# Kernel tuning notes

Measured on AMD Instinct MI355X. Metric: run time of the kernel, lower is better.

The kernel has to match this reference:

```python
import jax, jax.numpy as jnp
import numpy as np
from jax import lax

DN = ('NCHW', 'OIHW', 'NCHW')
BETA = 0.25


def _conv(x, w, b, stride, pad):
    y = lax.conv_general_dilated(x, w, (stride, stride), [(pad, pad), (pad, pad)],
                                 dimension_numbers=DN)
    return y + b[None, :, None, None]


def _convT(x, w, b, stride, pad, opad):
    # torch ConvTranspose2d(w: [in,out,kh,kw]) == dilated conv with flipped, transposed kernel
    k = w.shape[2]
    wf = jnp.transpose(w, (1, 0, 2, 3))[:, :, ::-1, ::-1]
    lo = k - 1 - pad
    hi = k - 1 - pad + opad
    y = lax.conv_general_dilated(x, wf, (1, 1), [(lo, hi), (lo, hi)],
                                 lhs_dilation=(stride, stride), dimension_numbers=DN)
    return y + b[None, :, None, None]


def setup_inputs() -> dict:
    key = jax.random.key(0)
    ks = jax.random.split(key, 16)
    s = 0.05
    inp = {
        'x': jax.random.normal(ks[0], (64, 3, 125, 125), jnp.float32),
        'enc_w1': jax.random.normal(ks[1], (32, 3, 3, 3), jnp.float32) * s,
        'enc_b1': jnp.zeros((32,), jnp.float32),
        'enc_w2': jax.random.normal(ks[2], (64, 32, 3, 3), jnp.float32) * s,
        'enc_b2': jnp.zeros((64,), jnp.float32),
        'enc_w3': jax.random.normal(ks[3], (64, 64, 1, 1), jnp.float32) * s,
        'enc_b3': jnp.zeros((64,), jnp.float32),
        'codebook': jax.random.normal(ks[4], (512, 64), jnp.float32),
        'dec_w1': jax.random.normal(ks[5], (64, 64, 3, 3), jnp.float32) * s,  # torch [in,out,kh,kw]
        'dec_b1': jnp.zeros((64,), jnp.float32),
        'dec_w2': jax.random.normal(ks[6], (64, 32, 3, 3), jnp.float32) * s,
        'dec_b2': jnp.zeros((32,), jnp.float32),
        'dec_w3': jax.random.normal(ks[7], (32, 3, 2, 2), jnp.float32) * s,
        'dec_b3': jnp.zeros((3,), jnp.float32),
    }
    return inp


def reference(x, enc_w1, enc_b1, enc_w2, enc_b2, enc_w3, enc_b3, codebook,
              dec_w1, dec_b1, dec_w2, dec_b2, dec_w3, dec_b3):
    # Encoder
    z = jax.nn.relu(_conv(x, enc_w1, enc_b1, 2, 1))
    z = jax.nn.relu(_conv(z, enc_w2, enc_b2, 2, 1))
    z = _conv(z, enc_w3, enc_b3, 1, 0)  # [B, D, h, w]

    # VQ (training mode)
    zp = jnp.transpose(z, (0, 2, 3, 1))  # [B, h, w, D]
    flat = zp.reshape(-1, zp.shape[-1])  # [N, D]
    d = (jnp.sum(flat * flat, axis=1, keepdims=True)
         + jnp.sum(codebook * codebook, axis=1)
         - 2.0 * flat @ codebook.T)  # [N, K]
    idx = jnp.argmin(d, axis=1)
    q = codebook[idx].reshape(zp.shape)

    q_latent_loss = jnp.mean((q - lax.stop_gradient(zp)) ** 2)
    e_latent_loss = jnp.mean((zp - lax.stop_gradient(q)) ** 2)
    e_q_loss = q_latent_loss + BETA * e_latent_loss

    q_st = zp + lax.stop_gradient(q - zp)  # straight-through
    e = jnp.transpose(q_st, (0, 3, 1, 2))

    # Decoder
    h = jax.nn.relu(_convT(e, dec_w1, dec_b1, 2, 1, 1))
    h = jax.nn.relu(_convT(h, dec_w2, dec_b2, 2, 1, 1))
    x_recon = _convT(h, dec_w3, dec_b3, 1, 2, 0)

    recon_loss = jnp.sum((x_recon - x) ** 2)
    loss_sum = e_q_loss + recon_loss
    return (loss_sum, e_q_loss, recon_loss, x_recon)
```

## Files before the change

### kernel.cpp

```cpp
#include <hip/hip_runtime.h>

#define DEV __device__ __forceinline__
typedef unsigned short u16;
typedef __bf16 bf16x8 __attribute__((ext_vector_type(8)));
typedef float f32x4 __attribute__((ext_vector_type(4)));

DEV u16 f2bf(float f) {
  unsigned u = __float_as_uint(f);
  u += 0x7FFF + ((u >> 16) & 1);
  return (u16)(u >> 16);
}


__global__ __launch_bounds__(256) void k_prep(
    const float* __restrict__ ew1, const float* __restrict__ ew2,
    const float* __restrict__ ew3, const float* __restrict__ dw1,
    const float* __restrict__ dw2, const float* __restrict__ dw3,
    const float* __restrict__ cb,
    float* __restrict__ wc1p, float* __restrict__ wc3p,
    u16* __restrict__ w3f, float* __restrict__ c2,
    u16* __restrict__ w2f, u16* __restrict__ wt1f, u16* __restrict__ wt2f,
    u16* __restrict__ cbf) {
  int i = blockIdx.x * 256 + threadIdx.x;
  if (i < 864) {
    int cl = i & 7; int t = i >> 3; int tap = t % 9; t /= 9; int ci = t % 3; int cog = t / 3;
    wc1p[i] = ew1[((cog * 8 + cl) * 3 + ci) * 9 + tap];
  } else if (i < 4960) {
    int j = i - 864; int cl = j & 7; int t = j >> 3; int ci = t & 63; int cog = t >> 6;
    wc3p[j] = ew3[(cog * 8 + cl) * 64 + ci];
  } else if (i < 9056) {
    int j = i - 4960;
    int jj = j & 7; int lane = (j >> 3) & 63; int tp = (j >> 9) & 3; int hl = j >> 11;
    int kh = tp >> 1, kw = tp & 1;
    int ci = ((lane >> 4) << 3) + jj; int co = lane & 15;
    float wv = (co < 3) ? dw3[((ci * 3 + co) * 2 + kh) * 2 + kw] : 0.f;
    u16 hi = f2bf(wv);
    if (hl == 0) w3f[j] = hi;
    else         w3f[j] = f2bf(wv - __uint_as_float((unsigned)hi << 16));
  } else if (i < 9568) {
    int k = i - 9056;
    const float4* c4 = (const float4*)(cb + (k << 6));
    float s = 0.f;
    #pragma unroll
    for (int q = 0; q < 16; ++q) { float4 v = c4[q]; s += v.x*v.x + v.y*v.y + v.z*v.z + v.w*v.w; }
    c2[k] = s;
  } else if (i < 28000) {
    int j = i - 9568;
    int jj = j & 7; int lane = (j >> 3) & 63; int nf = (j >> 9) & 3; int kt = j >> 11;
    int kh = kt / 3, kw = kt % 3;
    int ci = ((lane >> 4) << 3) + jj; int co = (nf << 4) + (lane & 15);
    w2f[j] = f2bf(ew2[((co * 32 + ci) * 3 + kh) * 3 + kw]);
  } else if (i < 64864) {
    int j = i - 28000;
    int jj = j & 7; int lane = (j >> 3) & 63; int nf = (j >> 9) & 3; int s = (j >> 11) & 1; int kt = j >> 12;
    int kh = kt / 3, kw = kt % 3;
    int ci = (s << 5) + ((lane >> 4) << 3) + jj; int co = (nf << 4) + (lane & 15);
    wt1f[j] = f2bf(dw1[((ci * 64 + co) * 3 + kh) * 3 + kw]);
  } else if (i < 83296) {
    int j = i - 64864;
    int jj = j & 7; int lane = (j >> 3) & 63; int nf = (j >> 9) & 1; int s = (j >> 10) & 1; int kt = j >> 11;
    int kh = kt / 3, kw = kt % 3;
    int ci = (s << 5) + ((lane >> 4) << 3) + jj; int co = (nf << 4) + (lane & 15);
    wt2f[j] = f2bf(dw2[((ci * 32 + co) * 3 + kh) * 3 + kw]);
  } else if (i < 148832) {
    int j = i - 83296;
    int jj = j & 7; int lane = (j >> 3) & 63; int nt = (j >> 9) & 31; int ks = (j >> 14) & 1; int hl = j >> 15;
    int ci = (ks << 5) + ((lane >> 4) << 3) + jj;
    int code = (nt << 4) + (lane & 15);
    float v = cb[(code << 6) + ci];
    u16 hi = f2bf(v);
    cbf[j] = hl ? f2bf(v - __uint_as_float((unsigned)hi << 16)) : hi;
  }
}

__global__ __launch_bounds__(256) void k_pad(
    const float* __restrict__ x, float* __restrict__ xp) {
  int idx = blockIdx.x * 256 + threadIdx.x;
  int c4 = idx & 31;
  int r  = (idx >> 5) % 129;
  int cbp = (idx >> 5) / 129;
  int ih = r - 1;
  float4 v = make_float4(0.f, 0.f, 0.f, 0.f);
  if ((unsigned)ih < 125u) {
    const float* rp = x + (cbp * 125 + ih) * 125;
    int iw0 = c4 * 4 - 1;
    if (iw0 >= 0)        v.x = rp[iw0];
    if (iw0 + 1 < 125)   v.y = rp[iw0 + 1];
    if (iw0 + 2 < 125)   v.z = rp[iw0 + 2];
    if (iw0 + 3 < 125)   v.w = rp[iw0 + 3];
  }
  *(float4*)(xp + (cbp * 129 + r) * 128 + c4 * 4) = v;
}

__global__ __launch_bounds__(256) void k_conv1(
    const float* __restrict__ xp, const float* __restrict__ wp,
    const float* __restrict__ bias, u16* __restrict__ z1t) {
  __shared__ u16 st[256 * 34];
  int t = threadIdx.x;
  int slab = blockIdx.x & 15, b = blockIdx.x >> 4;
  int tx = t & 15, ty = (t >> 4) & 3, cg = t >> 6;
  int oh = slab * 4 + ty;
  int co0 = cg * 8;
  const float* wcg = wp + cg * 216;
  float acc[8][4];
  #pragma unroll
  for (int c = 0; c < 8; ++c) {
    float bv = bias[co0 + c];
    #pragma unroll
    for (int s = 0; s < 4; ++s) acc[c][s] = bv;
  }
  #pragma unroll
  for (int ci = 0; ci < 3; ++ci) {
    #pragma unroll
    for (int kh = 0; kh < 3; ++kh) {
      const float* rp = xp + ((b * 3 + ci) * 129 + (2 * oh + kh)) * 128 + 8 * tx;
      float4 qa = *(const float4*)rp;
      float4 qb = *(const float4*)(rp + 4);
      float v8 = rp[8];
      float v[9] = {qa.x, qa.y, qa.z, qa.w, qb.x, qb.y, qb.z, qb.w, v8};
      #pragma unroll
      for (int kw = 0; kw < 3; ++kw) {
        const float* wq = wcg + (ci * 9 + kh * 3 + kw) * 8;
        float4 wa = *(const float4*)wq;
        float4 wb = *(const float4*)(wq + 4);
        float w8[8] = {wa.x, wa.y, wa.z, wa.w, wb.x, wb.y, wb.z, wb.w};
        #pragma unroll
        for (int s = 0; s < 4; ++s) {
          float in = v[2 * s + kw];
          #pragma unroll
          for (int c = 0; c < 8; ++c) acc[c][s] = fmaf(in, w8[c], acc[c][s]);
        }
      }
    }
  }
  #pragma unroll
  for (int s = 0; s < 4; ++s) {
    bool wok = (tx * 4 + s) < 63;
    unsigned p0 = 0, p1 = 0, p2 = 0, p3 = 0;
    if (wok) {
      p0 = f2bf(fmaxf(acc[0][s], 0.f)) | ((unsigned)f2bf(fmaxf(acc[1][s], 0.f)) << 16);
      p1 = f2bf(fmaxf(acc[2][s], 0.f)) | ((unsigned)f2bf(fmaxf(acc[3][s], 0.f)) << 16);
      p2 = f2bf(fmaxf(acc[4][s], 0.f)) | ((unsigned)f2bf(fmaxf(acc[5][s], 0.f)) << 16);
      p3 = f2bf(fmaxf(acc[6][s], 0.f)) | ((unsigned)f2bf(fmaxf(acc[7][s], 0.f)) << 16);
    }
    int lpix = tx * 16 + ty * 4 + s;
    *(uint4*)&st[lpix * 34 + co0] = make_uint4(p0, p1, p2, p3);
  }
  __syncthreads();
  {
    int p = t;
    int ow = (p >> 4) * 4 + (p & 3);
    int ohl = (p >> 2) & 3;
    int oho = slab * 4 + ohl;
    if (oho < 63) {
      const u16* lp = &st[p * 34];
      uint4 a0 = *(const uint4*)(lp);
      uint4 a1 = *(const uint4*)(lp + 8);
      uint4 a2 = *(const uint4*)(lp + 16);
      uint4 a3 = *(const uint4*)(lp + 24);
      uint4* gp = (uint4*)(z1t + ((b * 63 + oho) * 64 + ow) * 32);
      gp[0] = a0; gp[1] = a1; gp[2] = a2; gp[3] = a3;
    }
  }
}

__global__ __launch_bounds__(256) void k_conv2(
    const u16* __restrict__ z1t, const u16* __restrict__ wf,
    const float* __restrict__ bias, float* __restrict__ z2) {
  int t = threadIdx.x;
  int lane = t & 63, wv = t >> 6;
  int n = lane & 15, q = lane >> 4;
  int raw = blockIdx.x;
  int wg = ((raw & 7) << 8) + (raw >> 3);
  int oh = wg & 31, b = wg >> 5;
  int xt = wv & 1, ch = wv >> 1;
  int xA = xt * 16 + n;
  f32x4 acc[2] = {{0,0,0,0},{0,0,0,0}};
  #pragma unroll
  for (int kh = 0; kh < 3; ++kh) {
    int ih = 2 * oh - 1 + kh;
    bool yok = (unsigned)ih < 63u;
    #pragma unroll
    for (int kw = 0; kw < 3; ++kw) {
      int iw = 2 * xA - 1 + kw;
      bool ok = yok && (iw >= 0);
      bf16x8 a = {};
      if (ok) a = *(const bf16x8*)(z1t + ((b * 63 + ih) * 64 + iw) * 32 + q * 8);
      int kt = kh * 3 + kw;
      const u16* wb = wf + ((kt << 2) + (ch << 1)) * 512 + lane * 8;
      bf16x8 b0 = *(const bf16x8*)wb;
      bf16x8 b1 = *(const bf16x8*)(wb + 512);
      acc[0] = __builtin_amdgcn_mfma_f32_16x16x32_bf16(a, b0, acc[0], 0, 0, 0);
      acc[1] = __builtin_amdgcn_mfma_f32_16x16x32_bf16(a, b1, acc[1], 0, 0, 0);
    }
  }
  #pragma unroll
  for (int j = 0; j < 2; ++j) {
    int co = ((ch << 1) + j) * 16 + n;
    float bv = bias[co];
    float4 rv = make_float4(fmaxf(acc[j][0] + bv, 0.f), fmaxf(acc[j][1] + bv, 0.f),
                            fmaxf(acc[j][2] + bv, 0.f), fmaxf(acc[j][3] + bv, 0.f));
    *(float4*)(z2 + ((b * 64 + co) * 32 + oh) * 32 + xt * 16 + q * 4) = rv;
  }
}

__global__ __launch_bounds__(256) void k_conv3(
    const float* __restrict__ in, const float* __restrict__ wp,
    const float* __restrict__ bias, float* __restrict__ z3,
    u16* __restrict__ z3h, u16* __restrict__ z3l) {
  __shared__ u16 lh[128 * 72];
  __shared__ u16 ll[128 * 72];
  int t = threadIdx.x;
  int pxg = blockIdx.x & 7; int b = blockIdx.x >> 3;
  int pxi = t & 31, cog = t >> 5;
  int px0 = pxg * 128 + pxi * 4;
  const float* wcg = wp + cog * 512;
  int co0 = cog * 8;
  float acc[8][4];
  #pragma unroll
  for (int c = 0; c < 8; ++c) {
    float bv = bias[co0 + c];
    #pragma unroll
    for (int s = 0; s < 4; ++s) acc[c][s] = bv;
  }
  const float* ip = in + (b << 16) + px0;
  for (int ci = 0; ci < 64; ++ci) {
    float4 v = *(const float4*)(ip + (ci << 10));
    float4 wa = *(const float4*)(wcg + ci * 8);
    float4 wb = *(const float4*)(wcg + ci * 8 + 4);
    float w8[8] = {wa.x, wa.y, wa.z, wa.w, wb.x, wb.y, wb.z, wb.w};
    #pragma unroll
    for (int c = 0; c < 8; ++c) {
      acc[c][0] = fmaf(v.x, w8[c], acc[c][0]);
      acc[c][1] = fmaf(v.y, w8[c], acc[c][1]);
      acc[c][2] = fmaf(v.z, w8[c], acc[c][2]);
      acc[c][3] = fmaf(v.w, w8[c], acc[c][3]);
    }
  }
  float* op = z3 + ((b << 6) + co0) * 1024 + px0;
  #pragma unroll
  for (int c = 0; c < 8; ++c)
    *(float4*)(op + (c << 10)) = make_float4(acc[c][0], acc[c][1], acc[c][2], acc[c][3]);
  #pragma unroll
  for (int s = 0; s < 4; ++s) {
    unsigned h[4], l[4];
    #pragma unroll
    for (int g = 0; g < 4; ++g) {
      float v0 = acc[2 * g][s], v1 = acc[2 * g + 1][s];
      u16 h0 = f2bf(v0), h1 = f2bf(v1);
      u16 l0 = f2bf(v0 - __uint_as_float((unsigned)h0 << 16));
      u16 l1 = f2bf(v1 - __uint_as_float((unsigned)h1 << 16));
      h[g] = h0 | ((unsigned)h1 << 16);
      l[g] = l0 | ((unsigned)l1 << 16);
    }
    int la = (pxi * 4 + s) * 72 + co0;
    *(uint4*)&lh[la] = make_uint4(h[0], h[1], h[2], h[3]);
    *(uint4*)&ll[la] = make_uint4(l[0], l[1], l[2], l[3]);
  }
  __syncthreads();
  {
    int p = t >> 1, half = t & 1;
    int la = p * 72 + half * 32;
    uint4 h0 = *(uint4*)&lh[la],      h1 = *(uint4*)&lh[la + 8];
    uint4 h2 = *(uint4*)&lh[la + 16], h3 = *(uint4*)&lh[la + 24];
    uint4 l0 = *(uint4*)&ll[la],      l1 = *(uint4*)&ll[la + 8];
    uint4 l2 = *(uint4*)&ll[la + 16], l3 = *(uint4*)&ll[la + 24];
    long gp = ((long)b * 1024 + pxg * 128 + p) * 64 + half * 32;
    uint4* oh = (uint4*)(z3h + gp);
    uint4* ol = (uint4*)(z3l + gp);
    oh[0] = h0; oh[1] = h1; oh[2] = h2; oh[3] = h3;
    ol[0] = l0; ol[1] = l1; ol[2] = l2; ol[3] = l3;
  }
}

__global__ __launch_bounds__(256) void k_vqp(
    const u16* __restrict__ z3h, const u16* __restrict__ z3l,
    const u16* __restrict__ cbf, const float* __restrict__ c2v,
    int* __restrict__ idxb) {
  int t = threadIdx.x;
  int lane = t & 63, wv = t >> 6;
  int n = lane & 15, q = lane >> 4;
  int p0 = blockIdx.x * 64;
  bf16x8 Ah[4][2], Al[4][2];
  #pragma unroll
  for (int mt = 0; mt < 4; ++mt) {
    const u16* ap = z3h + (p0 + mt * 16 + n) * 64 + q * 8;
    const u16* al = z3l + (p0 + mt * 16 + n) * 64 + q * 8;
    Ah[mt][0] = *(const bf16x8*)ap;  Ah[mt][1] = *(const bf16x8*)(ap + 32);
    Al[mt][0] = *(const bf16x8*)al;  Al[mt][1] = *(const bf16x8*)(al + 32);
  }
  float bs[4][4]; int bix[4][4];
  #pragma unroll
  for (int mt = 0; mt < 4; ++mt)
    #pragma unroll
    for (int r = 0; r < 4; ++r) { bs[mt][r] = 3.4e38f; bix[mt][r] = 0; }
  #pragma unroll
  for (int nt0 = 0; nt0 < 8; ++nt0) {
    int nt = wv * 8 + nt0;
    const u16* bp = cbf + lane * 8;
    bf16x8 Bh0 = *(const bf16x8*)(bp + (nt << 9));
    bf16x8 Bh1 = *(const bf16x8*)(bp + ((32 + nt) << 9));
    bf16x8 Bl0 = *(const bf16x8*)(bp + ((64 + nt) << 9));
    bf16x8 Bl1 = *(const bf16x8*)(bp + ((96 + nt) << 9));
    float c2 = c2v[(nt << 4) + n];
    #pragma unroll
    for (int mt = 0; mt < 4; ++mt) {
      f32x4 acc = {0.f, 0.f, 0.f, 0.f};
      acc = __builtin_amdgcn_mfma_f32_16x16x32_bf16(Ah[mt][0], Bh0, acc, 0, 0, 0);
      acc = __builtin_amdgcn_mfma_f32_16x16x32_bf16(Ah[mt][1], Bh1, acc, 0, 0, 0);
      acc = __builtin_amdgcn_mfma_f32_16x16x32_bf16(Al[mt][0], Bh0, acc, 0, 0, 0);
      acc = __builtin_amdgcn_mfma_f32_16x16x32_bf16(Al[mt][1], Bh1, acc, 0, 0, 0);
      acc = __builtin_amdgcn_mfma_f32_16x16x32_bf16(Ah[mt][0], Bl0, acc, 0, 0, 0);
      acc = __builtin_amdgcn_mfma_f32_16x16x32_bf16(Ah[mt][1], Bl1, acc, 0, 0, 0);
      int idx = (nt << 4) + n;
      #pragma unroll
      for (int r = 0; r < 4; ++r) {
        float sc = fmaf(-2.f, acc[r], c2);
        if (sc < bs[mt][r]) { bs[mt][r] = sc; bix[mt][r] = idx; }
      }
    }
  }
  #pragma unroll
  for (int off = 8; off > 0; off >>= 1) {
    #pragma unroll
    for (int mt = 0; mt < 4; ++mt)
      #pragma unroll
      for (int r = 0; r < 4; ++r) {
        float os = __shfl_xor(bs[mt][r], off, 16);
        int oi = __shfl_xor(bix[mt][r], off, 16);
        if (os < bs[mt][r] || (os == bs[mt][r] && oi < bix[mt][r])) {
          bs[mt][r] = os; bix[mt][r] = oi;
        }
      }
  }
  __shared__ float ls[4][64];
  __shared__ int   li[4][64];
  if (n == 0) {
    #pragma unroll
    for (int mt = 0; mt < 4; ++mt)
      #pragma unroll
      for (int r = 0; r < 4; ++r) {
        int px = mt * 16 + q * 4 + r;
        ls[wv][px] = bs[mt][r];
        li[wv][px] = bix[mt][r];
      }
  }
  __syncthreads();
  if (t < 64) {
    float best = ls[0][t]; int bi = li[0][t];
    #pragma unroll
    for (int w = 1; w < 4; ++w) {
      float s = ls[w][t]; int ii = li[w][t];
      if (s < best || (s == best && ii < bi)) { best = s; bi = ii; }
    }
    idxb[p0 + t] = bi;
  }
}

__global__ __launch_bounds__(256) void k_vqf(
    const float* __restrict__ z3, const float* __restrict__ cb,
    const int* __restrict__ idxb, u16* __restrict__ et,
    float* __restrict__ acc) {
  int n = blockIdx.x * 256 + threadIdx.x;
  int bi = idxb[n];
  int b = n >> 10, hw = n & 1023;
  const float* zp = z3 + (b << 16) + hw;
  uint2* ep = (uint2*)(et + (n << 6));
  const float4* cq = (const float4*)(cb + (bi << 6));
  float lsum = 0.f;
  #pragma unroll
  for (int i = 0; i < 16; ++i) {
    float4 c = cq[i];
    float zv, df;
    zv = zp[(4*i+0) << 10]; df = c.x - zv; lsum = fmaf(df, df, lsum);
    zv = zp[(4*i+1) << 10]; df = c.y - zv; lsum = fmaf(df, df, lsum);
    zv = zp[(4*i+2) << 10]; df = c.z - zv; lsum = fmaf(df, df, lsum);
    zv = zp[(4*i+3) << 10]; df = c.w - zv; lsum = fmaf(df, df, lsum);
    ep[i] = make_uint2(f2bf(c.x) | ((unsigned)f2bf(c.y) << 16),
                       f2bf(c.z) | ((unsigned)f2bf(c.w) << 16));
  }
  __shared__ float red[256];
  red[threadIdx.x] = lsum; __syncthreads();
  #pragma unroll
  for (int s = 128; s > 0; s >>= 1) {
    if (threadIdx.x < s) red[threadIdx.x] += red[threadIdx.x + s];
    __syncthreads();
  }
  if (threadIdx.x == 0) atomicAdd(acc + 0, red[0]);
}

__global__ __launch_bounds__(256) void k_convT1(
    const u16* __restrict__ et, const u16* __restrict__ wf,
    const float* __restrict__ bias, u16* __restrict__ h1t) {
  __shared__ u16 wl[36 * 512];
  __shared__ u16 st[4][64 * 34];
  int t = threadIdx.x;
  int lane = t & 63, wv = t >> 6;
  int yw = wv & 1, xt = wv >> 1;
  int raw = blockIdx.x;
  int wg = ((raw & 7) << 7) + (raw >> 3);
  int cog = wg & 1;
  int yg = (wg >> 1) & 7;
  int b = wg >> 4;
  {
    const uint4* gw = (const uint4*)wf;
    uint4* lw = (uint4*)wl;
    #pragma unroll
    for (int k = 0; k < 9; ++k) {
      int i = t + 256 * k;
      int slot = i >> 6, within = i & 63;
      int kt = slot >> 2, j = (slot >> 1) & 1, ks = slot & 1;
      int goff = (kt << 12) + (((ks << 2) + (cog << 1) + j) << 9);
      lw[i] = gw[(goff >> 3) + within];
    }
  }
  int n = lane & 15, q = lane >> 4;
  int m = xt * 16 + n;
  __syncthreads();
  for (int iter = 0; iter < 2; ++iter) {
    int y = yg * 4 + iter * 2 + yw;
    const u16* base0 = et + (((b * 32 + y) * 32) << 6) + q * 8;
    bf16x8 P00a, P00b, P01a = {}, P01b = {}, P10a = {}, P10b = {}, P11a = {}, P11b = {};
    { const u16* p = base0 + (m << 6); P00a = *(const bf16x8*)p; P00b = *(const bf16x8*)(p + 32); }
    if (m + 1 < 32) { const u16* p = base0 + ((m + 1) << 6); P01a = *(const bf16x8*)p; P01b = *(const bf16x8*)(p + 32); }
    if (y + 1 < 32) {
      const u16* base1 = base0 + (32 << 6);
      { const u16* p = base1 + (m << 6); P10a = *(const bf16x8*)p; P10b = *(const bf16x8*)(p + 32); }
      if (m + 1 < 32) { const u16* p = base1 + ((m + 1) << 6); P11a = *(const bf16x8*)p; P11b = *(const bf16x8*)(p + 32); }
    }
    f32x4 accE[2][2] = {};
    f32x4 accO[2][2] = {};
    #pragma unroll
    for (int kw = 0; kw < 3; ++kw) {
      int pwi = (kw == 1) ? 0 : 1;
      bf16x8 A0a = (kw == 0) ? P01a : P00a;
      bf16x8 A0b = (kw == 0) ? P01b : P00b;
      bf16x8 A1a = (kw == 0) ? P11a : P10a;
      bf16x8 A1b = (kw == 0) ? P11b : P10b;
      #pragma unroll
      for (int j = 0; j < 2; ++j) {
        const u16* wE  = wl + ((((3 + kw) << 2) + (j << 1)) << 9) + lane * 8;
        const u16* wO0 = wl + (((kw << 2) + (j << 1)) << 9) + lane * 8;
        const u16* wO2 = wl + ((((6 + kw) << 2) + (j << 1)) << 9) + lane * 8;
        bf16x8 bE0 = *(const bf16x8*)wE;
        bf16x8 bE1 = *(const bf16x8*)(wE + 512);
        accE[j][pwi] = __builtin_amdgcn_mfma_f32_16x16x32_bf16(A0a, bE0, accE[j][pwi], 0, 0, 0);
        accE[j][pwi] = __builtin_amdgcn_mfma_f32_16x16x32_bf16(A0b, bE1, accE[j][pwi], 0, 0, 0);
        bf16x8 bO00 = *(const bf16x8*)wO0;
        bf16x8 bO01 = *(const bf16x8*)(wO0 + 512);
        accO[j][pwi] = __builtin_amdgcn_mfma_f32_16x16x32_bf16(A1a, bO00, accO[j][pwi], 0, 0, 0);
        accO[j][pwi] = __builtin_amdgcn_mfma_f32_16x16x32_bf16(A1b, bO01, accO[j][pwi], 0, 0, 0);
        bf16x8 bO20 = *(const bf16x8*)wO2;
        bf16x8 bO21 = *(const bf16x8*)(wO2 + 512);
        accO[j][pwi] = __builtin_amdgcn_mfma_f32_16x16x32_bf16(A0a, bO20, accO[j][pwi], 0, 0, 0);
        accO[j][pwi] = __builtin_amdgcn_mfma_f32_16x16x32_bf16(A0b, bO21, accO[j][pwi], 0, 0, 0);
      }
    }
    #pragma unroll
    for (int j = 0; j < 2; ++j) {
      int col = j * 16 + n;
      float bv = bias[cog * 32 + col];
      #pragma unroll
      for (int pw = 0; pw < 2; ++pw)
        #pragma unroll
        for (int r = 0; r < 4; ++r) {
          int ow = 2 * (xt * 16 + q * 4 + r) + pw;
          st[yw * 2 + 0][ow * 34 + col] = f2bf(fmaxf(accE[j][pw][r] + bv, 0.f));
          st[yw * 2 + 1][ow * 34 + col] = f2bf(fmaxf(accO[j][pw][r] + bv, 0.f));
        }
    }
    __syncthreads();
    {
      int row = t >> 6, ow = t & 63;
      const u16* lp = &st[row][ow * 34];
      uint4* gp = (uint4*)(h1t + (((b * 64 + yg * 8 + iter * 4 + row) * 64 + ow) << 6) + cog * 32);
      gp[0] = *(const uint4*)(lp);
      gp[1] = *(const uint4*)(lp + 8);
      gp[2] = *(const uint4*)(lp + 16);
      gp[3] = *(const uint4*)(lp + 24);
    }
    __syncthreads();
  }
}

__global__ __launch_bounds__(256) void k_convT2(
    const u16* __restrict__ h1t, const u16* __restrict__ wf,
    const float* __restrict__ bias, u16* __restrict__ h2t) {
  __shared__ u16 wl[18432];
  __shared__ u16 st[2][128 * 34];
  int t = threadIdx.x;
  int lane = t & 63, xt = t >> 6;
  int n = lane & 15, q = lane >> 4;
  int raw = blockIdx.x;
  int wg = ((raw & 7) << 7) + (raw >> 3);
  int yg = wg & 15, b = wg >> 4;
  {
    const uint4* gw = (const uint4*)wf;
    uint4* lw = (uint4*)wl;
    #pragma unroll
    for (int k = 0; k < 9; ++k) lw[t + 256 * k] = gw[t + 256 * k];
  }
  int m = xt * 16 + n;
  __syncthreads();
  for (int yp = 0; yp < 4; ++yp) {
    int y = yg * 4 + yp;
    const u16* base0 = h1t + (((b * 64 + y) * 64) << 6) + q * 8;
    bf16x8 P00a, P00b, P01a = {}, P01b = {}, P10a = {}, P10b = {}, P11a = {}, P11b = {};
    { const u16* p = base0 + (m << 6); P00a = *(const bf16x8*)p; P00b = *(const bf16x8*)(p + 32); }
    if (m + 1 < 64) { const u16* p = base0 + ((m + 1) << 6); P01a = *(const bf16x8*)p; P01b = *(const bf16x8*)(p + 32); }
    if (y + 1 < 64) {
      const u16* base1 = base0 + (64 << 6);
      { const u16* p = base1 + (m << 6); P10a = *(const bf16x8*)p; P10b = *(const bf16x8*)(p + 32); }
      if (m + 1 < 64) { const u16* p = base1 + ((m + 1) << 6); P11a = *(const bf16x8*)p; P11b = *(const bf16x8*)(p + 32); }
    }
    f32x4 accE[2][2] = {};
    f32x4 accO[2][2] = {};
    #pragma unroll
    for (int kw = 0; kw < 3; ++kw) {
      int pwi = (kw == 1) ? 0 : 1;
      bf16x8 A0a = (kw == 0) ? P01a : P00a;
      bf16x8 A0b = (kw == 0) ? P01b : P00b;
      bf16x8 A1a = (kw == 0) ? P11a : P10a;
      bf16x8 A1b = (kw == 0) ? P11b : P10b;
      const u16* wbE = wl + ((3 + kw) << 11) + lane * 8;
      const u16* wbO0 = wl + (kw << 11) + lane * 8;
      const u16* wbO2 = wl + ((6 + kw) << 11) + lane * 8;
      #pragma unroll
      for (int nf = 0; nf < 2; ++nf) {
        bf16x8 bE0 = *(const bf16x8*)(wbE + nf * 512);
        bf16x8 bE1 = *(const bf16x8*)(wbE + (2 + nf) * 512);
        accE[nf][pwi] = __builtin_amdgcn_mfma_f32_16x16x32_bf16(A0a, bE0, accE[nf][pwi], 0, 0, 0);
        accE[nf][pwi] = __builtin_amdgcn_mfma_f32_16x16x32_bf16(A0b, bE1, accE[nf][pwi], 0, 0, 0);
        bf16x8 bO00 = *(const bf16x8*)(wbO0 + nf * 512);
        bf16x8 bO01 = *(const bf16x8*)(wbO0 + (2 + nf) * 512);
        accO[nf][pwi] = __builtin_amdgcn_mfma_f32_16x16x32_bf16(A1a, bO00, accO[nf][pwi], 0, 0, 0);
        accO[nf][pwi] = __builtin_amdgcn_mfma_f32_16x16x32_bf16(A1b, bO01, accO[nf][pwi], 0, 0, 0);
        bf16x8 bO20 = *(const bf16x8*)(wbO2 + nf * 512);
        bf16x8 bO21 = *(const bf16x8*)(wbO2 + (2 + nf) * 512);
        accO[nf][pwi] = __builtin_amdgcn_mfma_f32_16x16x32_bf16(A0a, bO20, accO[nf][pwi], 0, 0, 0);
        accO[nf][pwi] = __builtin_amdgcn_mfma_f32_16x16x32_bf16(A0b, bO21, accO[nf][pwi], 0, 0, 0);
      }
    }
    #pragma unroll
    for (int nf = 0; nf < 2; ++nf) {
      int co = nf * 16 + n;
      float bv = bias[co];
      #pragma unroll
      for (int pw = 0; pw < 2; ++pw)
        #pragma unroll
        for (int r = 0; r < 4; ++r) {
          int ow = 2 * (xt * 16 + q * 4 + r) + pw;
          st[0][ow * 34 + co] = f2bf(fmaxf(accE[nf][pw][r] + bv, 0.f));
          st[1][ow * 34 + co] = f2bf(fmaxf(accO[nf][pw][r] + bv, 0.f));
        }
    }
    __syncthreads();
    {
      int ow = t >> 1, sg = t & 1;
      #pragma unroll
      for (int l = 0; l < 2; ++l) {
        const u16* lp = &st[l][ow * 34 + sg * 16];
        unsigned w0 = *(const unsigned*)(lp + 0), w1 = *(const unsigned*)(lp + 2);
        unsigned w2 = *(const unsigned*)(lp + 4), w3 = *(const unsigned*)(lp + 6);
        unsigned w4 = *(const unsigned*)(lp + 8), w5 = *(const unsigned*)(lp + 10);
        unsigned w6 = *(const unsigned*)(lp + 12), w7 = *(const unsigned*)(lp + 14);
        uint4* gp = (uint4*)(h2t + ((((b * 128 + yg * 8 + yp * 2 + l) * 128) + ow) << 5) + sg * 16);
        gp[0] = make_uint4(w0, w1, w2, w3);
        gp[1] = make_uint4(w4, w5, w6, w7);
      }
    }
    __syncthreads();
  }
}

__global__ __launch_bounds__(256) void k_convT3(
    const u16* __restrict__ h2t, const u16* __restrict__ w3f,
    const float* __restrict__ bias, const float* __restrict__ x,
    float* __restrict__ xr, float* __restrict__ psum) {
  int t = threadIdx.x;
  int lane = t & 63, wv = t >> 6;
  int n = lane & 15, q = lane >> 4;
  int raw = blockIdx.x;
  int wg = ((raw & 7) << 8) + (raw >> 3);
  int rg = wg & 31, b = wg >> 5;
  int oh0 = rg * 4;
  const u16* wbp = w3f + lane * 8;
  bf16x8 Bh0 = *(const bf16x8*)(wbp);
  bf16x8 Bh1 = *(const bf16x8*)(wbp + 512);
  bf16x8 Bh2 = *(const bf16x8*)(wbp + 1024);
  bf16x8 Bh3 = *(const bf16x8*)(wbp + 1536);
  bf16x8 Bl0 = *(const bf16x8*)(wbp + 2048);
  bf16x8 Bl1 = *(const bf16x8*)(wbp + 2560);
  bf16x8 Bl2 = *(const bf16x8*)(wbp + 3072);
  bf16x8 Bl3 = *(const bf16x8*)(wbp + 3584);
  float bv = (n < 3) ? bias[n] : 0.f;
  float lsum = 0.f;
  for (int r4 = 0; r4 < 4; ++r4) {
    int oh = oh0 + r4;
    if (oh < 125) {
      const u16* row1 = h2t + (((long)b * 128 + (oh + 1)) << 12) + q * 8;
      const u16* row2 = row1 + 4096;
      #pragma unroll
      for (int ti = 0; ti < 2; ++ti) {
        int tt = wv + ti * 4;
        int c1 = tt * 16 + n + 1;
        int c2 = c1 + 1;
        bf16x8 a11 = {}, a12 = {}, a21 = {}, a22 = {};
        if (c1 < 128) { a11 = *(const bf16x8*)(row1 + (c1 << 5));
                        a21 = *(const bf16x8*)(row2 + (c1 << 5)); }
        if (c2 < 128) { a12 = *(const bf16x8*)(row1 + (c2 << 5));
                        a22 = *(const bf16x8*)(row2 + (c2 << 5)); }
        f32x4 acc = {0.f, 0.f, 0.f, 0.f};
        acc = __builtin_amdgcn_mfma_f32_16x16x32_bf16(a11, Bh3, acc, 0, 0, 0);
        acc = __builtin_amdgcn_mfma_f32_16x16x32_bf16(a12, Bh2, acc, 0, 0, 0);
        acc = __builtin_amdgcn_mfma_f32_16x16x32_bf16(a21, Bh1, acc, 0, 0, 0);
        acc = __builtin_amdgcn_mfma_f32_16x16x32_bf16(a22, Bh0, acc, 0, 0, 0);
        acc = __builtin_amdgcn_mfma_f32_16x16x32_bf16(a11, Bl3, acc, 0, 0, 0);
        acc = __builtin_amdgcn_mfma_f32_16x16x32_bf16(a12, Bl2, acc, 0, 0, 0);
        acc = __builtin_amdgcn_mfma_f32_16x16x32_bf16(a21, Bl1, acc, 0, 0, 0);
        acc = __builtin_amdgcn_mfma_f32_16x16x32_bf16(a22, Bl0, acc, 0, 0, 0);
        if (n < 3) {
          int ow0 = tt * 16 + q * 4;
          int o = b * 46875 + n * 15625 + oh * 125 + ow0;
          if (ow0 + 3 < 125) {
            float4 v = make_float4(acc[0] + bv, acc[1] + bv, acc[2] + bv, acc[3] + bv);
            float4 xv = *(const float4*)(x + o);
            *(float4*)(xr + o) = v;
            float d0 = v.x - xv.x, d1 = v.y - xv.y, d2 = v.z - xv.z, d3 = v.w - xv.w;
            lsum += d0 * d0 + d1 * d1 + d2 * d2 + d3 * d3;
          } else {
            #pragma unroll
            for (int r = 0; r < 4; ++r) {
              if (ow0 + r < 125) {
                float v = acc[r] + bv;
                xr[o + r] = v;
                float d = v - x[o + r];
                lsum = fmaf(d, d, lsum);
              }
            }
          }
        }
      }
    }
  }
  __shared__ float red[256];
  red[t] = lsum; __syncthreads();
  #pragma unroll
  for (int s = 128; s > 0; s >>= 1) {
    if (t < s) red[t] += red[t + s];
    __syncthreads();
  }
  if (t == 0) psum[raw] = red[0];
}

__global__ __launch_bounds__(256) void k_fin(
    const float* __restrict__ acc, const float* __restrict__ psum,
    float* __restrict__ out) {
  int t = threadIdx.x;
  float s = 0.f;
  for (int i = t; i < 2048; i += 256) s += psum[i];
  __shared__ float red[256];
  red[t] = s; __syncthreads();
  #pragma unroll
  for (int k = 128; k > 0; k >>= 1) {
    if (t < k) red[t] += red[t + k];
    __syncthreads();
  }
  if (t == 0) {
    float eq  = 1.25f * acc[0] / 4194304.0f;
    float rec = red[0];
    out[0] = eq + rec;
    out[1] = eq;
    out[2] = rec;
  }
}

extern "C" void kernel_launch(void* const* d_in, const int* in_sizes, int n_in,
                              void* d_out, int out_size, void* d_ws, size_t ws_size,
                              hipStream_t stream) {
  (void)in_sizes; (void)n_in; (void)out_size; (void)ws_size;
  const float* x   = (const float*)d_in[0];
  const float* ew1 = (const float*)d_in[1];
  const float* eb1 = (const float*)d_in[2];
  const float* ew2 = (const float*)d_in[3];
  const float* eb2 = (const float*)d_in[4];
  const float* ew3 = (const float*)d_in[5];
  const float* eb3 = (const float*)d_in[6];
  const float* cb  = (const float*)d_in[7];
  const float* dw1 = (const float*)d_in[8];
  const float* db1 = (const float*)d_in[9];
  const float* dw2 = (const float*)d_in[10];
  const float* db2 = (const float*)d_in[11];
  const float* dw3 = (const float*)d_in[12];
  const float* db3 = (const float*)d_in[13];
  float* out = (float*)d_out;
  char*  ws  = (char*)d_ws;

  float*  acc  = (float*)(ws + 0);
  float*  c2   = (float*)(ws + 256);
  float*  wc1p = (float*)(ws + 4096);
  float*  wc3p = (float*)(ws + 8192);
  u16*    w3f  = (u16*)  (ws + 24576);
  u16*    w2f  = (u16*)  (ws + 36864);
  u16*    wt1f = (u16*)  (ws + 73728);
  u16*    wt2f = (u16*)  (ws + 147456);
  float*  psum = (float*)(ws + 184320);
  u16*    cbf  = (u16*)  (ws + 262144);
  u16*    z1t  = (u16*)  (ws + 1048576);
  float*  z2   = (float*)(ws + 18874368);
  float*  z3   = (float*)(ws + 35651584);
  int*    idxb = (int*)  (ws + 52428800);
  u16*    et   = (u16*)  (ws + 54525952);
  u16*    h1t  = (u16*)  (ws + 1048576);
  u16*    h2t  = (u16*)  (ws + 67108864);
  u16*    z3h  = (u16*)  (ws + 134217728);
  u16*    z3l  = (u16*)  (ws + 142606336);
  float*  xp   = (float*)(ws + 150994944);

  hipMemsetAsync(acc, 0, 64, stream);
  k_prep  <<<582,  256, 0, stream>>>(ew1, ew2, ew3, dw1, dw2, dw3, cb,
                                     wc1p, wc3p, w3f, c2, w2f, wt1f, wt2f, cbf);
  k_pad   <<<3096, 256, 0, stream>>>(x, xp);
  k_conv1 <<<1024, 256, 0, stream>>>(xp, wc1p, eb1, z1t);
  k_conv2 <<<2048, 256, 0, stream>>>(z1t, w2f, eb2, z2);
  k_conv3 <<<512,  256, 0, stream>>>(z2, wc3p, eb3, z3, z3h, z3l);
  k_vqp   <<<1024, 256, 0, stream>>>(z3h, z3l, cbf, c2, idxb);
  k_vqf   <<<256,  256, 0, stream>>>(z3, cb, idxb, et, acc);
  k_convT1<<<1024, 256, 0, stream>>>(et, wt1f, db1, h1t);
  k_convT2<<<1024, 256, 0, stream>>>(h1t, wt2f, db2, h2t);
  k_convT3<<<2048, 256, 0, stream>>>(h2t, w3f, db3, x, out + 3, psum);
  k_fin   <<<1,    256, 0, stream>>>(acc, psum, out);
}
```

Measured before the change: 289.5 us.

## Fuse pad into prep, VQ gather into argmin, and final reduction into convT3

Merges the input padding kernel into the weight-prep launch as extra blocks, folds the codebook gather, latent-loss and bf16 embedding write into the VQ argmin kernel, and replaces the final one-block reduction with atomics and a last-block-done counter in convT3. This cuts three kernel launches and the round trip of the index buffer through global memory. In exchange it adds atomic contention and a fence in convT3 and makes the float summation order nondeterministic. It also removes the unroll pragma from the codebook tile loop in the VQ kernel.

```diff
diff --git a/kernel.cpp b/kernel.cpp
--- a/kernel.cpp
+++ b/kernel.cpp
@@ -20,7 +20,26 @@
     float* __restrict__ wc1p, float* __restrict__ wc3p,
     u16* __restrict__ w3f, float* __restrict__ c2,
     u16* __restrict__ w2f, u16* __restrict__ wt1f, u16* __restrict__ wt2f,
-    u16* __restrict__ cbf) {
+    u16* __restrict__ cbf,
+    const float* __restrict__ x, float* __restrict__ xp) {
+  if (blockIdx.x >= 582) {
+    int idx = (blockIdx.x - 582) * 256 + threadIdx.x;
+    int c4 = idx & 31;
+    int r  = (idx >> 5) % 129;
+    int cbp = (idx >> 5) / 129;
+    int ih = r - 1;
+    float4 v = make_float4(0.f, 0.f, 0.f, 0.f);
+    if ((unsigned)ih < 125u) {
+      const float* rp = x + (cbp * 125 + ih) * 125;
+      int iw0 = c4 * 4 - 1;
+      if (iw0 >= 0)        v.x = rp[iw0];
+      if (iw0 + 1 < 125)   v.y = rp[iw0 + 1];
+      if (iw0 + 2 < 125)   v.z = rp[iw0 + 2];
+      if (iw0 + 3 < 125)   v.w = rp[iw0 + 3];
+    }
+    *(float4*)(xp + (cbp * 129 + r) * 128 + c4 * 4) = v;
+    return;
+  }
   int i = blockIdx.x * 256 + threadIdx.x;
   if (i < 864) {
     int cl = i & 7; int t = i >> 3; int tap = t % 9; t /= 9; int ci = t % 3; int cog = t / 3;
@@ -73,25 +92,6 @@
   }
 }
 
-__global__ __launch_bounds__(256) void k_pad(
-    const float* __restrict__ x, float* __restrict__ xp) {
-  int idx = blockIdx.x * 256 + threadIdx.x;
-  int c4 = idx & 31;
-  int r  = (idx >> 5) % 129;
-  int cbp = (idx >> 5) / 129;
-  int ih = r - 1;
-  float4 v = make_float4(0.f, 0.f, 0.f, 0.f);
-  if ((unsigned)ih < 125u) {
-    const float* rp = x + (cbp * 125 + ih) * 125;
-    int iw0 = c4 * 4 - 1;
-    if (iw0 >= 0)        v.x = rp[iw0];
-    if (iw0 + 1 < 125)   v.y = rp[iw0 + 1];
-    if (iw0 + 2 < 125)   v.z = rp[iw0 + 2];
-    if (iw0 + 3 < 125)   v.w = rp[iw0 + 3];
-  }
-  *(float4*)(xp + (cbp * 129 + r) * 128 + c4 * 4) = v;
-}
-
 __global__ __launch_bounds__(256) void k_conv1(
     const float* __restrict__ xp, const float* __restrict__ wp,
     const float* __restrict__ bias, u16* __restrict__ z1t) {
@@ -273,10 +273,11 @@
   }
 }
 
-__global__ __launch_bounds__(256) void k_vqp(
+__global__ __launch_bounds__(256) void k_vqpf(
     const u16* __restrict__ z3h, const u16* __restrict__ z3l,
     const u16* __restrict__ cbf, const float* __restrict__ c2v,
-    int* __restrict__ idxb) {
+    const float* __restrict__ z3, const float* __restrict__ cb,
+    u16* __restrict__ et, float* __restrict__ acc) {
   int t = threadIdx.x;
   int lane = t & 63, wv = t >> 6;
   int n = lane & 15, q = lane >> 4;
@@ -294,7 +295,6 @@
   for (int mt = 0; mt < 4; ++mt)
     #pragma unroll
     for (int r = 0; r < 4; ++r) { bs[mt][r] = 3.4e38f; bix[mt][r] = 0; }
-  #pragma unroll
   for (int nt0 = 0; nt0 < 8; ++nt0) {
     int nt = wv * 8 + nt0;
     const u16* bp = cbf + lane * 8;
@@ -305,17 +305,17 @@
     float c2 = c2v[(nt << 4) + n];
     #pragma unroll
     for (int mt = 0; mt < 4; ++mt) {
-      f32x4 acc = {0.f, 0.f, 0.f, 0.f};
-      acc = __builtin_amdgcn_mfma_f32_16x16x32_bf16(Ah[mt][0], Bh0, acc, 0, 0, 0);
-      acc = __builtin_amdgcn_mfma_f32_16x16x32_bf16(Ah[mt][1], Bh1, acc, 0, 0, 0);
-      acc = __builtin_amdgcn_mfma_f32_16x16x32_bf16(Al[mt][0], Bh0, acc, 0, 0, 0);
-      acc = __builtin_amdgcn_mfma_f32_16x16x32_bf16(Al[mt][1], Bh1, acc, 0, 0, 0);
-      acc = __builtin_amdgcn_mfma_f32_16x16x32_bf16(Ah[mt][0], Bl0, acc, 0, 0, 0);
-      acc = __builtin_amdgcn_mfma_f32_16x16x32_bf16(Ah[mt][1], Bl1, acc, 0, 0, 0);
+      f32x4 a = {0.f, 0.f, 0.f, 0.f};
+      a = __builtin_amdgcn_mfma_f32_16x16x32_bf16(Ah[mt][0], Bh0, a, 0, 0, 0);
+      a = __builtin_amdgcn_mfma_f32_16x16x32_bf16(Ah[mt][1], Bh1, a, 0, 0, 0);
+      a = __builtin_amdgcn_mfma_f32_16x16x32_bf16(Al[mt][0], Bh0, a, 0, 0, 0);
+      a = __builtin_amdgcn_mfma_f32_16x16x32_bf16(Al[mt][1], Bh1, a, 0, 0, 0);
+      a = __builtin_amdgcn_mfma_f32_16x16x32_bf16(Ah[mt][0], Bl0, a, 0, 0, 0);
+      a = __builtin_amdgcn_mfma_f32_16x16x32_bf16(Ah[mt][1], Bl1, a, 0, 0, 0);
       int idx = (nt << 4) + n;
       #pragma unroll
       for (int r = 0; r < 4; ++r) {
-        float sc = fmaf(-2.f, acc[r], c2);
+        float sc = fmaf(-2.f, a[r], c2);
         if (sc < bs[mt][r]) { bs[mt][r] = sc; bix[mt][r] = idx; }
       }
     }
@@ -335,6 +335,7 @@
   }
   __shared__ float ls[4][64];
   __shared__ int   li[4][64];
+  __shared__ int   lfin[64];
   if (n == 0) {
     #pragma unroll
     for (int mt = 0; mt < 4; ++mt)
@@ -353,40 +354,40 @@
       float s = ls[w][t]; int ii = li[w][t];
       if (s < best || (s == best && ii < bi)) { best = s; bi = ii; }
     }
-    idxb[p0 + t] = bi;
-  }
-}
-
-__global__ __launch_bounds__(256) void k_vqf(
-    const float* __restrict__ z3, const float* __restrict__ cb,
-    const int* __restrict__ idxb, u16* __restrict__ et,
-    float* __restrict__ acc) {
-  int n = blockIdx.x * 256 + threadIdx.x;
-  int bi = idxb[n];
-  int b = n >> 10, hw = n & 1023;
-  const float* zp = z3 + (b << 16) + hw;
-  uint2* ep = (uint2*)(et + (n << 6));
-  const float4* cq = (const float4*)(cb + (bi << 6));
+    lfin[t] = bi;
+  }
+  __syncthreads();
+  int pxl = t >> 2, ciq = t & 3;
+  int ng = p0 + pxl;
+  int bb = ng >> 10, hw = ng & 1023;
+  int bi = lfin[pxl];
+  const float* zp = z3 + (bb << 16) + hw;
+  const float4* cq = (const float4*)(cb + (bi << 6) + (ciq << 4));
   float lsum = 0.f;
-  #pragma unroll
-  for (int i = 0; i < 16; ++i) {
+  unsigned pk[8];
+  #pragma unroll
+  for (int i = 0; i < 4; ++i) {
     float4 c = cq[i];
+    int cbase = (ciq << 4) + (i << 2);
     float zv, df;
-    zv = zp[(4*i+0) << 10]; df = c.x - zv; lsum = fmaf(df, df, lsum);
-    zv = zp[(4*i+1) << 10]; df = c.y - zv; lsum = fmaf(df, df, lsum);
-    zv = zp[(4*i+2) << 10]; df = c.z - zv; lsum = fmaf(df, df, lsum);
-    zv = zp[(4*i+3) << 10]; df = c.w - zv; lsum = fmaf(df, df, lsum);
-    ep[i] = make_uint2(f2bf(c.x) | ((unsigned)f2bf(c.y) << 16),
-                       f2bf(c.z) | ((unsigned)f2bf(c.w) << 16));
-  }
+    zv = zp[(cbase + 0) << 10]; df = c.x - zv; lsum = fmaf(df, df, lsum);
+    zv = zp[(cbase + 1) << 10]; df = c.y - zv; lsum = fmaf(df, df, lsum);
+    zv = zp[(cbase + 2) << 10]; df = c.z - zv; lsum = fmaf(df, df, lsum);
+    zv = zp[(cbase + 3) << 10]; df = c.w - zv; lsum = fmaf(df, df, lsum);
+    pk[2 * i]     = f2bf(c.x) | ((unsigned)f2bf(c.y) << 16);
+    pk[2 * i + 1] = f2bf(c.z) | ((unsigned)f2bf(c.w) << 16);
+  }
+  uint4* ep = (uint4*)(et + ((long)ng << 6) + (ciq << 4));
+  ep[0] = make_uint4(pk[0], pk[1], pk[2], pk[3]);
+  ep[1] = make_uint4(pk[4], pk[5], pk[6], pk[7]);
   __shared__ float red[256];
-  red[threadIdx.x] = lsum; __syncthreads();
+  red[t] = lsum; __syncthreads();
   #pragma unroll
   for (int s = 128; s > 0; s >>= 1) {
-    if (threadIdx.x < s) red[threadIdx.x] += red[threadIdx.x + s];
+    if (t < s) red[t] += red[t + s];
     __syncthreads();
   }
-  if (threadIdx.x == 0) atomicAdd(acc + 0, red[0]);
+  if (t == 0) atomicAdd(acc + 0, red[0]);
 }
 
 __global__ __launch_bounds__(256) void k_convT1(
@@ -576,7 +577,7 @@
 __global__ __launch_bounds__(256) void k_convT3(
     const u16* __restrict__ h2t, const u16* __restrict__ w3f,
     const float* __restrict__ bias, const float* __restrict__ x,
-    float* __restrict__ xr, float* __restrict__ psum) {
+    float* __restrict__ xr, float* __restrict__ acc, float* __restrict__ out) {
   int t = threadIdx.x;
   int lane = t & 63, wv = t >> 6;
   int n = lane & 15, q = lane >> 4;
@@ -610,20 +611,20 @@
                         a21 = *(const bf16x8*)(row2 + (c1 << 5)); }
         if (c2 < 128) { a12 = *(const bf16x8*)(row1 + (c2 << 5));
                         a22 = *(const bf16x8*)(row2 + (c2 << 5)); }
-        f32x4 acc = {0.f, 0.f, 0.f, 0.f};
-        acc = __builtin_amdgcn_mfma_f32_16x16x32_bf16(a11, Bh3, acc, 0, 0, 0);
-        acc = __builtin_amdgcn_mfma_f32_16x16x32_bf16(a12, Bh2, acc, 0, 0, 0);
-        acc = __builtin_amdgcn_mfma_f32_16x16x32_bf16(a21, Bh1, acc, 0, 0, 0);
-        acc = __builtin_amdgcn_mfma_f32_16x16x32_bf16(a22, Bh0, acc, 0, 0, 0);
-        acc = __builtin_amdgcn_mfma_f32_16x16x32_bf16(a11, Bl3, acc, 0, 0, 0);
-        acc = __builtin_amdgcn_mfma_f32_16x16x32_bf16(a12, Bl2, acc, 0, 0, 0);
-        acc = __builtin_amdgcn_mfma_f32_16x16x32_bf16(a21, Bl1, acc, 0, 0, 0);
-        acc = __builtin_amdgcn_mfma_f32_16x16x32_bf16(a22, Bl0, acc, 0, 0, 0);
+        f32x4 a = {0.f, 0.f, 0.f, 0.f};
+        a = __builtin_amdgcn_mfma_f32_16x16x32_bf16(a11, Bh3, a, 0, 0, 0);
+        a = __builtin_amdgcn_mfma_f32_16x16x32_bf16(a12, Bh2, a, 0, 0, 0);
+        a = __builtin_amdgcn_mfma_f32_16x16x32_bf16(a21, Bh1, a, 0, 0, 0);
+        a = __builtin_amdgcn_mfma_f32_16x16x32_bf16(a22, Bh0, a, 0, 0, 0);
+        a = __builtin_amdgcn_mfma_f32_16x16x32_bf16(a11, Bl3, a, 0, 0, 0);
+        a = __builtin_amdgcn_mfma_f32_16x16x32_bf16(a12, Bl2, a, 0, 0, 0);
+        a = __builtin_amdgcn_mfma_f32_16x16x32_bf16(a21, Bl1, a, 0, 0, 0);
+        a = __builtin_amdgcn_mfma_f32_16x16x32_bf16(a22, Bl0, a, 0, 0, 0);
         if (n < 3) {
           int ow0 = tt * 16 + q * 4;
           int o = b * 46875 + n * 15625 + oh * 125 + ow0;
           if (ow0 + 3 < 125) {
-            float4 v = make_float4(acc[0] + bv, acc[1] + bv, acc[2] + bv, acc[3] + bv);
+            float4 v = make_float4(a[0] + bv, a[1] + bv, a[2] + bv, a[3] + bv);
             float4 xv = *(const float4*)(x + o);
             *(float4*)(xr + o) = v;
             float d0 = v.x - xv.x, d1 = v.y - xv.y, d2 = v.z - xv.z, d3 = v.w - xv.w;
@@ -632,7 +633,7 @@
             #pragma unroll
             for (int r = 0; r < 4; ++r) {
               if (ow0 + r < 125) {
-                float v = acc[r] + bv;
+                float v = a[r] + bv;
                 xr[o + r] = v;
                 float d = v - x[o + r];
                 lsum = fmaf(d, d, lsum);
@@ -650,28 +651,17 @@
     if (t < s) red[t] += red[t + s];
     __syncthreads();
   }
-  if (t == 0) psum[raw] = red[0];
-}
-
-__global__ __launch_bounds__(256) void k_fin(
-    const float* __restrict__ acc, const float* __restrict__ psum,
-    float* __restrict__ out) {
-  int t = threadIdx.x;
-  float s = 0.f;
-  for (int i = t; i < 2048; i += 256) s += psum[i];
-  __shared__ float red[256];
-  red[t] = s; __syncthreads();
-  #pragma unroll
-  for (int k = 128; k > 0; k >>= 1) {
-    if (t < k) red[t] += red[t + k];
-    __syncthreads();
-  }
   if (t == 0) {
-    float eq  = 1.25f * acc[0] / 4194304.0f;
-    float rec = red[0];
-    out[0] = eq + rec;
-    out[1] = eq;
-    out[2] = rec;
+    atomicAdd(acc + 1, red[0]);
+    __threadfence();
+    int done = atomicAdd((int*)acc + 2, 1);
+    if (done == 2047) {
+      float eq  = 1.25f * atomicAdd(acc + 0, 0.f) / 4194304.0f;
+      float rec = atomicAdd(acc + 1, 0.f);
+      out[0] = eq + rec;
+      out[1] = eq;
+      out[2] = rec;
+    }
   }
 }
 
@@ -704,12 +694,10 @@
   u16*    w2f  = (u16*)  (ws + 36864);
   u16*    wt1f = (u16*)  (ws + 73728);
   u16*    wt2f = (u16*)  (ws + 147456);
-  float*  psum = (float*)(ws + 184320);
   u16*    cbf  = (u16*)  (ws + 262144);
   u16*    z1t  = (u16*)  (ws + 1048576);
   float*  z2   = (float*)(ws + 18874368);
   float*  z3   = (float*)(ws + 35651584);
-  int*    idxb = (int*)  (ws + 52428800);
   u16*    et   = (u16*)  (ws + 54525952);
   u16*    h1t  = (u16*)  (ws + 1048576);
   u16*    h2t  = (u16*)  (ws + 67108864);
@@ -718,16 +706,14 @@
   float*  xp   = (float*)(ws + 150994944);
 
   hipMemsetAsync(acc, 0, 64, stream);
-  k_prep  <<<582,  256, 0, stream>>>(ew1, ew2, ew3, dw1, dw2, dw3, cb,
-                                     wc1p, wc3p, w3f, c2, w2f, wt1f, wt2f, cbf);
-  k_pad   <<<3096, 256, 0, stream>>>(x, xp);
+  k_prep  <<<3678, 256, 0, stream>>>(ew1, ew2, ew3, dw1, dw2, dw3, cb,
+                                     wc1p, wc3p, w3f, c2, w2f, wt1f, wt2f, cbf,
+                                     x, xp);
   k_conv1 <<<1024, 256, 0, stream>>>(xp, wc1p, eb1, z1t);
   k_conv2 <<<2048, 256, 0, stream>>>(z1t, w2f, eb2, z2);
   k_conv3 <<<512,  256, 0, stream>>>(z2, wc3p, eb3, z3, z3h, z3l);
-  k_vqp   <<<1024, 256, 0, stream>>>(z3h, z3l, cbf, c2, idxb);
-  k_vqf   <<<256,  256, 0, stream>>>(z3, cb, idxb, et, acc);
+  k_vqpf  <<<1024, 256, 0, stream>>>(z3h, z3l, cbf, c2, z3, cb, et, acc);
   k_convT1<<<1024, 256, 0, stream>>>(et, wt1f, db1, h1t);
   k_convT2<<<1024, 256, 0, stream>>>(h1t, wt2f, db2, h2t);
-  k_convT3<<<2048, 256, 0, stream>>>(h2t, w3f, db3, x, out + 3, psum);
-  k_fin   <<<1,    256, 0, stream>>>(acc, psum, out);
-}
+  k_convT3<<<2048, 256, 0, stream>>>(h2t, w3f, db3, x, out + 3, acc, out);
+}
```

Result: slower. 336.0 us (+16.1%).
